# Kernel tuning notes

Hardware: AMD Instinct MI355X
Metric: run time of the kernel (lower is better)

Reference implementation:

```python
import jax, jax.numpy as jnp
import numpy as np

D_MODEL, D_STATE, D_INNER, DT_RANK, K = 64, 16, 128, 4, 4
EPS = 1e-6  # RMSNorm eps


def setup_inputs() -> dict:
    key = jax.random.key(0)
    ks = jax.random.split(key, 12)
    B, L = 8, 4096
    s = 0.02
    x = jax.random.normal(ks[0], (B, L, D_MODEL), dtype=jnp.float32)
    w_norm = jnp.ones((D_MODEL,), jnp.float32)
    W_in = jax.random.normal(ks[1], (2 * D_INNER, D_MODEL), jnp.float32) * s
    b_in = jnp.zeros((2 * D_INNER,), jnp.float32)
    W_conv = jax.random.normal(ks[2], (D_INNER, D_INNER, K), jnp.float32) * s
    b_conv = jnp.zeros((D_INNER,), jnp.float32)
    W_xp = jax.random.normal(ks[3], (DT_RANK + 2 * D_STATE, D_INNER), jnp.float32) * s
    b_xp = jnp.zeros((DT_RANK + 2 * D_STATE,), jnp.float32)
    W_dt = jax.random.normal(ks[4], (D_INNER, DT_RANK), jnp.float32) * s
    b_dt = jnp.zeros((D_INNER,), jnp.float32)
    W_out = jax.random.normal(ks[5], (D_MODEL, D_INNER), jnp.float32) * s
    b_out = jnp.zeros((D_MODEL,), jnp.float32)
    A_log = jnp.log(jnp.tile(jnp.arange(1, D_STATE + 1, dtype=jnp.float32), (D_INNER, 1)))
    D_param = jnp.ones((D_INNER,), jnp.float32)
    return dict(x=x, w_norm=w_norm, W_in=W_in, b_in=b_in, W_conv=W_conv, b_conv=b_conv,
                W_xp=W_xp, b_xp=b_xp, W_dt=W_dt, b_dt=b_dt, W_out=W_out, b_out=b_out,
                A_log=A_log, D_param=D_param)


def _mamba_block(xn, W_in, b_in, W_conv, b_conv, W_xp, b_xp, W_dt, b_dt, W_out, b_out, A_log, D_param):
    B, L, _ = xn.shape
    xz = xn @ W_in.T + b_in                      # (B,L,2*d_inner)
    u, z = jnp.split(xz, 2, axis=-1)
    z = jax.nn.silu(z)
    # conv1d: NCH, causal-style pad (K-1) both sides then truncate to L
    uc = jax.lax.conv_general_dilated(
        u.transpose(0, 2, 1), W_conv, window_strides=(1,), padding=[(K - 1, K - 1)],
        dimension_numbers=("NCH", "OIH", "NCH"))[:, :, :L] + b_conv[None, :, None]
    u = jax.nn.silu(uc.transpose(0, 2, 1))       # (B,L,d_inner)
    xp = u @ W_xp.T + b_xp
    dt, Bm, Cm = jnp.split(xp, [DT_RANK, DT_RANK + D_STATE], axis=-1)
    delta = jax.nn.softplus(dt @ W_dt.T + b_dt)  # (B,L,d_inner)
    A = -jnp.exp(A_log)                          # (d_inner, n)
    A_bar = jnp.exp(jnp.einsum('bld,dn->bldn', delta, A))
    B_bar_x = jnp.einsum('bld,bln,bld->bldn', delta, Bm, u)

    def step(h, inp):
        a, bx, c = inp                           # (B,d,n),(B,d,n),(B,n)
        h = a * h + bx
        y = jnp.einsum('bdn,bn->bd', h, c)
        return h, y

    h0 = jnp.zeros((B, D_INNER, D_STATE), xn.dtype)
    xs = (A_bar.transpose(1, 0, 2, 3), B_bar_x.transpose(1, 0, 2, 3), Cm.transpose(1, 0, 2))
    _, ys = jax.lax.scan(step, h0, xs)           # (L,B,d_inner)
    y = ys.transpose(1, 0, 2) + D_param * u
    y = y * z
    return y @ W_out.T + b_out


def reference(x, w_norm, W_in, b_in, W_conv, b_conv, W_xp, b_xp, W_dt, b_dt, W_out, b_out, A_log, D_param):
    xn = x * jax.lax.rsqrt(jnp.mean(x * x, axis=-1, keepdims=True) + EPS) * w_norm
    return x + _mamba_block(xn, W_in, b_in, W_conv, b_conv, W_xp, b_xp, W_dt, b_dt, W_out, b_out, A_log, D_param)
```

## Files before the change

### kernel.cpp

```cpp
#include <hip/hip_runtime.h>
#include <math.h>

#define D_MODEL 64
#define D_STATE 16
#define D_INNER 128
#define DT_RANK 4
#define BB 8
#define LL 4096
#define NTOK (BB*LL)
#define EPSV 1e-6f
#define NCHUNK 64
#define LC (LL/NCHUNK)
#define PAD 136

typedef __attribute__((ext_vector_type(8))) short bf16x8;
typedef __attribute__((ext_vector_type(4))) float f32x4;

__device__ __forceinline__ float sig_(float v) { return 1.f / (1.f + __expf(-v)); }
__device__ __forceinline__ float softplus_(float v) {
    return (v > 20.f) ? v : __logf(1.f + __expf(v));
}
__device__ __forceinline__ unsigned short f2bf(float x) {
    unsigned int u = __float_as_uint(x);
    u += 0x7fff + ((u >> 16) & 1);
    return (unsigned short)(u >> 16);
}
__device__ __forceinline__ float bf2f(unsigned short u) {
    return __uint_as_float(((unsigned int)u) << 16);
}
__device__ __forceinline__ unsigned int pack2bf(float a, float b) {
    return (unsigned int)f2bf(a) | ((unsigned int)f2bf(b) << 16);
}

__global__ __launch_bounds__(256) void pack_all(
    const float* __restrict__ W_in, const float* __restrict__ w_norm,
    const float* __restrict__ W_conv, const float* __restrict__ W_xp,
    const float* __restrict__ W_out,
    unsigned short* __restrict__ Win_bf, unsigned short* __restrict__ Bp,
    unsigned short* __restrict__ Wxp_bf, unsigned short* __restrict__ Wout_bf)
{
    int i = blockIdx.x * 256 + threadIdx.x;
    if (i < 16384) {
        Win_bf[i] = f2bf(W_in[i] * w_norm[i & 63]);
    } else if (i < 81920) {
        int j = i - 16384;
        int kk = j >> 14, o = (j >> 7) & 127, c = j & 127;
        Bp[j] = f2bf(W_conv[o * 512 + c * 4 + kk]);
    } else if (i < 88064) {
        int j = i - 81920;
        Wxp_bf[j] = ((j >> 7) < 36) ? f2bf(W_xp[j]) : (unsigned short)0;
    } else if (i < 96256) {
        int j = i - 88064;
        Wout_bf[j] = f2bf(W_out[j]);
    }
}

__global__ __launch_bounds__(256) void k1_fused(
    const float* __restrict__ x, const unsigned short* __restrict__ Win_bf,
    const float* __restrict__ b_in,
    unsigned short* __restrict__ u_bf, unsigned short* __restrict__ z_bf)
{
    __shared__ unsigned short axs[64 * 72];
    int tid = threadIdx.x;
    int tb = blockIdx.x * 64;
    {
        int t = tid >> 2, qt = tid & 3;
        float4 v[4];
        float ss = 0.f;
        #pragma unroll
        for (int j = 0; j < 4; ++j) {
            v[j] = *(const float4*)&x[(tb + t) * 64 + qt * 16 + j * 4];
            ss += v[j].x*v[j].x + v[j].y*v[j].y + v[j].z*v[j].z + v[j].w*v[j].w;
        }
        ss += __shfl_xor(ss, 1, 64);
        ss += __shfl_xor(ss, 2, 64);
        float r = rsqrtf(ss * (1.f / 64.f) + EPSV);
        unsigned short tmp[16];
        #pragma unroll
        for (int j = 0; j < 4; ++j) {
            tmp[4*j+0] = f2bf(v[j].x * r); tmp[4*j+1] = f2bf(v[j].y * r);
            tmp[4*j+2] = f2bf(v[j].z * r); tmp[4*j+3] = f2bf(v[j].w * r);
        }
        *(bf16x8*)&axs[t * 72 + qt * 16]     = *(bf16x8*)&tmp[0];
        *(bf16x8*)&axs[t * 72 + qt * 16 + 8] = *(bf16x8*)&tmp[8];
    }
    __syncthreads();
    int wave = tid >> 6, lane = tid & 63;
    int quad = lane >> 4, l16 = lane & 15;
    f32x4 acc[16];
    #pragma unroll
    for (int nt = 0; nt < 16; ++nt) acc[nt] = (f32x4){0.f, 0.f, 0.f, 0.f};
    bf16x8 a0 = *(const bf16x8*)&axs[(wave * 16 + l16) * 72 + quad * 8];
    bf16x8 a1 = *(const bf16x8*)&axs[(wave * 16 + l16) * 72 + 32 + quad * 8];
    #pragma unroll
    for (int nt = 0; nt < 16; ++nt) {
        bf16x8 b0 = *(const bf16x8*)&Win_bf[(nt * 16 + l16) * 64 + quad * 8];
        bf16x8 b1 = *(const bf16x8*)&Win_bf[(nt * 16 + l16) * 64 + 32 + quad * 8];
        acc[nt] = __builtin_amdgcn_mfma_f32_16x16x32_bf16(a0, b0, acc[nt], 0, 0, 0);
        acc[nt] = __builtin_amdgcn_mfma_f32_16x16x32_bf16(a1, b1, acc[nt], 0, 0, 0);
    }
    #pragma unroll
    for (int nt = 0; nt < 16; ++nt) {
        int o = nt * 16 + l16;
        float bo = b_in[o];
        #pragma unroll
        for (int r = 0; r < 4; ++r) {
            int t = tb + wave * 16 + quad * 4 + r;
            float v = acc[nt][r] + bo;
            if (o < 128) u_bf[t * 128 + o] = f2bf(v);
            else         z_bf[t * 128 + (o - 128)] = f2bf(v * sig_(v));
        }
    }
}

__global__ __launch_bounds__(256) void k2k3a_fused(
    const unsigned short* __restrict__ u_bf, const unsigned short* __restrict__ Bp,
    const float* __restrict__ b_conv,
    const unsigned short* __restrict__ Wxp_bf, const float* __restrict__ b_xp,
    const float* __restrict__ W_dt, const float* __restrict__ b_dt,
    const float* __restrict__ A_log,
    unsigned short* __restrict__ u_cbf, unsigned short* __restrict__ delta_bf,
    float* __restrict__ Bm, float* __restrict__ Cm,
    float* __restrict__ P, float* __restrict__ Q)
{
    __shared__ unsigned short uls[64 * PAD];
    __shared__ unsigned short dls[64 * PAD];
    __shared__ float bls[64 * 16];
    __shared__ float dts[64][4];
    __shared__ float Wd[512];
    __shared__ float bds[128];
    int tid = threadIdx.x;
    if (tid < 128) *(float4*)&Wd[tid * 4] = *(const float4*)&W_dt[tid * 4];
    else if (tid < 160) *(float4*)&bds[(tid - 128) * 4] = *(const float4*)&b_dt[(tid - 128) * 4];
    int wave = tid >> 6, lane = tid & 63;
    int quad = lane >> 4, l16 = lane & 15;
    int tb = blockIdx.x * 64;
    int bbase = tb & ~4095;
    int t0 = tb + wave * 16;
    f32x4 acc[8];
    #pragma unroll
    for (int og = 0; og < 8; ++og) acc[og] = (f32x4){0.f, 0.f, 0.f, 0.f};
    int row_base = t0 + l16 - 3;
    #pragma unroll
    for (int kk = 0; kk < 4; ++kk) {
        int row = row_base + kk;
        #pragma unroll
        for (int cs = 0; cs < 4; ++cs) {
            int kbase = cs * 32 + quad * 8;
            bf16x8 a = {0,0,0,0,0,0,0,0};
            if (row >= bbase)
                a = *(const bf16x8*)&u_bf[row * 128 + kbase];
            #pragma unroll
            for (int og = 0; og < 8; ++og) {
                bf16x8 b = *(const bf16x8*)&Bp[kk * 16384 + (og * 16 + l16) * 128 + kbase];
                acc[og] = __builtin_amdgcn_mfma_f32_16x16x32_bf16(a, b, acc[og], 0, 0, 0);
            }
        }
    }
    #pragma unroll
    for (int og = 0; og < 8; ++og) {
        int o = og * 16 + l16;
        float bc = b_conv[o];
        #pragma unroll
        for (int r = 0; r < 4; ++r) {
            int tloc = wave * 16 + quad * 4 + r;
            float v = acc[og][r] + bc;
            unsigned short ub = f2bf(v * sig_(v));
            u_cbf[(tb + tloc) * 128 + o] = ub;
            uls[tloc * PAD + o] = ub;
        }
    }
    __syncthreads();
    f32x4 xacc[3];
    #pragma unroll
    for (int nt = 0; nt < 3; ++nt) xacc[nt] = (f32x4){0.f, 0.f, 0.f, 0.f};
    #pragma unroll
    for (int cs = 0; cs < 4; ++cs) {
        int kbase = cs * 32 + quad * 8;
        bf16x8 a = *(const bf16x8*)&uls[(wave * 16 + l16) * PAD + kbase];
        #pragma unroll
        for (int nt = 0; nt < 3; ++nt) {
            bf16x8 b = *(const bf16x8*)&Wxp_bf[(nt * 16 + l16) * 128 + kbase];
            xacc[nt] = __builtin_amdgcn_mfma_f32_16x16x32_bf16(a, b, xacc[nt], 0, 0, 0);
        }
    }
    #pragma unroll
    for (int nt = 0; nt < 3; ++nt) {
        int j = nt * 16 + l16;
        float bx = (j < 36) ? b_xp[j] : 0.f;
        #pragma unroll
        for (int r = 0; r < 4; ++r) {
            int tloc = wave * 16 + quad * 4 + r;
            int t = tb + tloc;
            float val = xacc[nt][r] + bx;
            if (j < 4) {
                dts[tloc][j] = val;
            } else if (j < 20) {
                Bm[t * 16 + (j - 4)] = val;
                bls[tloc * 16 + (j - 4)] = val;
            } else if (j < 36) {
                Cm[t * 16 + (j - 20)] = val;
            }
        }
    }
    __syncthreads();
    {
        int tokloc = tid >> 2, dgrp = tid & 3;
        float dt0 = dts[tokloc][0], dt1 = dts[tokloc][1],
              dt2 = dts[tokloc][2], dt3 = dts[tokloc][3];
        int g = tb + tokloc;
        #pragma unroll
        for (int d4 = 0; d4 < 8; ++d4) {
            int d = dgrp * 32 + d4 * 4;
            float4 w0 = *(const float4*)&Wd[(d + 0) * 4];
            float4 w1 = *(const float4*)&Wd[(d + 1) * 4];
            float4 w2 = *(const float4*)&Wd[(d + 2) * 4];
            float4 w3 = *(const float4*)&Wd[(d + 3) * 4];
            float4 bdv = *(const float4*)&bds[d];
            float4 r;
            r.x = softplus_(bdv.x + dt0*w0.x + dt1*w0.y + dt2*w0.z + dt3*w0.w);
            r.y = softplus_(bdv.y + dt0*w1.x + dt1*w1.y + dt2*w1.z + dt3*w1.w);
            r.z = softplus_(bdv.z + dt0*w2.x + dt1*w2.y + dt2*w2.z + dt3*w2.w);
            r.w = softplus_(bdv.w + dt0*w3.x + dt1*w3.y + dt2*w3.z + dt3*w3.w);
            uint2 pk; pk.x = pack2bf(r.x, r.y); pk.y = pack2bf(r.z, r.w);
            *(uint2*)&delta_bf[g * 128 + d] = pk;
            *(uint2*)&dls[tokloc * PAD + d] = pk;
        }
    }
    __syncthreads();
    {
        int d = tid >> 1;
        int nb = (tid & 1) * 8;
        float4 Av0 = *(const float4*)&A_log[d * 16 + nb];
        float4 Av1 = *(const float4*)&A_log[d * 16 + nb + 4];
        float A0 = -__expf(Av0.x), A1 = -__expf(Av0.y),
              A2 = -__expf(Av0.z), A3 = -__expf(Av0.w);
        float A4 = -__expf(Av1.x), A5 = -__expf(Av1.y),
              A6 = -__expf(Av1.z), A7 = -__expf(Av1.w);
        float P0=1.f,P1=1.f,P2=1.f,P3=1.f,P4=1.f,P5=1.f,P6=1.f,P7=1.f;
        float Q0=0.f,Q1=0.f,Q2=0.f,Q3=0.f,Q4=0.f,Q5=0.f,Q6=0.f,Q7=0.f;
        for (int t = 0; t < LC; ++t) {
            float dl = bf2f(dls[t * PAD + d]);
            float uu = bf2f(uls[t * PAD + d]);
            float4 bm0 = *(const float4*)&bls[t * 16 + nb];
            float4 bm1 = *(const float4*)&bls[t * 16 + nb + 4];
            float du = dl * uu;
            float a0 = __expf(dl * A0), a1 = __expf(dl * A1),
                  a2 = __expf(dl * A2), a3 = __expf(dl * A3);
            float a4 = __expf(dl * A4), a5 = __expf(dl * A5),
                  a6 = __expf(dl * A6), a7 = __expf(dl * A7);
            P0 *= a0; P1 *= a1; P2 *= a2; P3 *= a3;
            P4 *= a4; P5 *= a5; P6 *= a6; P7 *= a7;
            Q0 = a0 * Q0 + du * bm0.x; Q1 = a1 * Q1 + du * bm0.y;
            Q2 = a2 * Q2 + du * bm0.z; Q3 = a3 * Q3 + du * bm0.w;
            Q4 = a4 * Q4 + du * bm1.x; Q5 = a5 * Q5 + du * bm1.y;
            Q6 = a6 * Q6 + du * bm1.z; Q7 = a7 * Q7 + du * bm1.w;
        }
        int idx = blockIdx.x * 2048 + d * 16 + nb;
        *(float4*)&P[idx]     = (float4){P0, P1, P2, P3};
        *(float4*)&P[idx + 4] = (float4){P4, P5, P6, P7};
        *(float4*)&Q[idx]     = (float4){Q0, Q1, Q2, Q3};
        *(float4*)&Q[idx + 4] = (float4){Q4, Q5, Q6, Q7};
    }
}

__global__ __launch_bounds__(256) void k4b_carry(
    const float* __restrict__ P, const float* __restrict__ Q, float* __restrict__ Hinit)
{
    int tid = blockIdx.x * 256 + threadIdx.x;
    int b = tid >> 11, dn = tid & 2047;
    float carry = 0.f;
    for (int c0 = 0; c0 < NCHUNK; c0 += 8) {
        float p[8], q[8];
        #pragma unroll
        for (int j = 0; j < 8; ++j) {
            int idx = (b * NCHUNK + c0 + j) * 2048 + dn;
            p[j] = P[idx]; q[j] = Q[idx];
        }
        #pragma unroll
        for (int j = 0; j < 8; ++j) {
            int idx = (b * NCHUNK + c0 + j) * 2048 + dn;
            Hinit[idx] = carry;
            carry = p[j] * carry + q[j];
        }
    }
}

__global__ __launch_bounds__(256) void k4c5_fused(
    const unsigned short* __restrict__ delta_bf, const unsigned short* __restrict__ u_cbf,
    const float* __restrict__ Bm, const float* __restrict__ Cm,
    const unsigned short* __restrict__ z_bf, const float* __restrict__ A_log,
    const float* __restrict__ D_param, const float* __restrict__ Hinit,
    const unsigned short* __restrict__ Wout_bf, const float* __restrict__ b_out,
    const float* __restrict__ x, float* __restrict__ out)
{
    __shared__ unsigned short dls[LC * 128];
    __shared__ unsigned short uls[LC * 128];
    __shared__ float bls[LC * 16];
    __shared__ float cls[LC * 16];
    __shared__ unsigned short yzls[LC * PAD];
    int bid = blockIdx.x;
    int tid = threadIdx.x, lane = tid & 63;
    int g0 = bid * 64;
    for (int i = tid; i < LC * 16; i += 256) {
        int row = i >> 4, q = i & 15;
        *(float4*)&dls[row * 128 + q * 8] =
            *(const float4*)&delta_bf[(g0 + row) * 128 + q * 8];
        *(float4*)&uls[row * 128 + q * 8] =
            *(const float4*)&u_cbf[(g0 + row) * 128 + q * 8];
        *(float4*)&yzls[row * PAD + q * 8] =
            *(const float4*)&z_bf[(g0 + row) * 128 + q * 8];
    }
    for (int i = tid; i < LC * 4; i += 256) {
        int row = i >> 2, q = i & 3;
        *(float4*)&bls[row * 16 + q * 4] = *(const float4*)&Bm[(g0 + row) * 16 + q * 4];
        *(float4*)&cls[row * 16 + q * 4] = *(const float4*)&Cm[(g0 + row) * 16 + q * 4];
    }
    int d = tid >> 1;
    int nb = (tid & 1) * 8;
    float4 Av0 = *(const float4*)&A_log[d * 16 + nb];
    float4 Av1 = *(const float4*)&A_log[d * 16 + nb + 4];
    float A0 = -__expf(Av0.x), A1 = -__expf(Av0.y), A2 = -__expf(Av0.z), A3 = -__expf(Av0.w);
    float A4 = -__expf(Av1.x), A5 = -__expf(Av1.y), A6 = -__expf(Av1.z), A7 = -__expf(Av1.w);
    int hbase = bid * 2048 + d * 16 + nb;
    float4 h0 = *(const float4*)&Hinit[hbase];
    float4 h1 = *(const float4*)&Hinit[hbase + 4];
    float Dp = D_param[d];
    __syncthreads();
    for (int t = 0; t < LC; ++t) {
        float dl = bf2f(dls[t * 128 + d]);
        float uu = bf2f(uls[t * 128 + d]);
        float4 bm0 = *(const float4*)&bls[t * 16 + nb];
        float4 bm1 = *(const float4*)&bls[t * 16 + nb + 4];
        float4 cm0 = *(const float4*)&cls[t * 16 + nb];
        float4 cm1 = *(const float4*)&cls[t * 16 + nb + 4];
        float du = dl * uu;
        float a0 = __expf(dl * A0), a1 = __expf(dl * A1),
              a2 = __expf(dl * A2), a3 = __expf(dl * A3);
        float a4 = __expf(dl * A4), a5 = __expf(dl * A5),
              a6 = __expf(dl * A6), a7 = __expf(dl * A7);
        h0.x = a0 * h0.x + du * bm0.x; h0.y = a1 * h0.y + du * bm0.y;
        h0.z = a2 * h0.z + du * bm0.z; h0.w = a3 * h0.w + du * bm0.w;
        h1.x = a4 * h1.x + du * bm1.x; h1.y = a5 * h1.y + du * bm1.y;
        h1.z = a6 * h1.z + du * bm1.z; h1.w = a7 * h1.w + du * bm1.w;
        float yv = h0.x * cm0.x + h0.y * cm0.y + h0.z * cm0.z + h0.w * cm0.w
                 + h1.x * cm1.x + h1.y * cm1.y + h1.z * cm1.z + h1.w * cm1.w;
        yv += __shfl_xor(yv, 1, 64);
        if ((tid & 1) == 0) {
            float y = yv + Dp * uu;
            y *= bf2f(yzls[t * PAD + d]);
            yzls[t * PAD + d] = f2bf(y);
        }
    }
    __syncthreads();
    int wave = tid >> 6;
    int quad = lane >> 4, l16 = lane & 15;
    f32x4 oacc[4];
    #pragma unroll
    for (int nt = 0; nt < 4; ++nt) oacc[nt] = (f32x4){0.f, 0.f, 0.f, 0.f};
    #pragma unroll
    for (int cs = 0; cs < 4; ++cs) {
        int kbase = cs * 32 + quad * 8;
        bf16x8 a = *(const bf16x8*)&yzls[(wave * 16 + l16) * PAD + kbase];
        #pragma unroll
        for (int nt = 0; nt < 4; ++nt) {
            bf16x8 bb = *(const bf16x8*)&Wout_bf[(nt * 16 + l16) * 128 + kbase];
            oacc[nt] = __builtin_amdgcn_mfma_f32_16x16x32_bf16(a, bb, oacc[nt], 0, 0, 0);
        }
    }
    #pragma unroll
    for (int nt = 0; nt < 4; ++nt) {
        int m = nt * 16 + l16;
        float bo = b_out[m];
        #pragma unroll
        for (int r = 0; r < 4; ++r) {
            int t = g0 + wave * 16 + quad * 4 + r;
            out[t * 64 + m] = oacc[nt][r] + bo + x[t * 64 + m];
        }
    }
}

extern "C" void kernel_launch(void* const* d_in, const int* in_sizes, int n_in,
                              void* d_out, int out_size, void* d_ws, size_t ws_size,
                              hipStream_t stream)
{
    const float* x       = (const float*)d_in[0];
    const float* w_norm  = (const float*)d_in[1];
    const float* W_in    = (const float*)d_in[2];
    const float* b_in    = (const float*)d_in[3];
    const float* W_conv  = (const float*)d_in[4];
    const float* b_conv  = (const float*)d_in[5];
    const float* W_xp    = (const float*)d_in[6];
    const float* b_xp    = (const float*)d_in[7];
    const float* W_dt    = (const float*)d_in[8];
    const float* b_dt    = (const float*)d_in[9];
    const float* W_out   = (const float*)d_in[10];
    const float* b_out   = (const float*)d_in[11];
    const float* A_log   = (const float*)d_in[12];
    const float* D_param = (const float*)d_in[13];
    float* ws = (float*)d_ws;

    unsigned short* u_bf = (unsigned short*)ws;
    unsigned short* z_bf = (unsigned short*)(ws + 2097152);
    unsigned short* u_cbf= (unsigned short*)(ws + 4194304);
    unsigned short* delta_bf = (unsigned short*)(ws + 6291456);
    float* Bm     = ws + 10485760;
    float* Cm     = ws + 11010048;
    float* P      = ws + 11534336;
    float* Q      = ws + 12582912;
    float* Hinit  = ws + 13631488;
    unsigned short* Bp      = (unsigned short*)(ws + 14680064);
    unsigned short* Wxp_bf  = (unsigned short*)(ws + 14712832);
    unsigned short* Wout_bf = (unsigned short*)(ws + 14715904);
    unsigned short* Win_bf  = (unsigned short*)(ws + 14720000);
    float* out    = (float*)d_out;

    pack_all<<<376, 256, 0, stream>>>(W_in, w_norm, W_conv, W_xp, W_out,
                                      Win_bf, Bp, Wxp_bf, Wout_bf);
    k1_fused<<<512, 256, 0, stream>>>(x, Win_bf, b_in, u_bf, z_bf);
    k2k3a_fused<<<512, 256, 0, stream>>>(u_bf, Bp, b_conv, Wxp_bf, b_xp,
                                         W_dt, b_dt, A_log,
                                         u_cbf, delta_bf, Bm, Cm, P, Q);
    k4b_carry<<<64, 256, 0, stream>>>(P, Q, Hinit);
    k4c5_fused<<<512, 256, 0, stream>>>(delta_bf, u_cbf, Bm, Cm, z_bf, A_log,
                                        D_param, Hinit, Wout_bf, b_out, x, out);
}
```

Baseline: 184.0 us.

## Double threads per block and split work across 8 waves in all main kernels

Raises block size from 256 to 512 threads in the three main kernels. Work is remapped so each wave covers half the output columns (GEMM tiles) and each scan thread handles 4 states instead of 8, with an extra shuffle reduction. The aim is more parallelism, since only 512 blocks are launched and the per-thread serial scan chains were long. The cost is more shuffles, more redundant A-fragment loads across waves, and uneven xp tile work between the two wave halves.

```diff
diff --git a/kernel.cpp b/kernel.cpp
--- a/kernel.cpp
+++ b/kernel.cpp
@@ -55,7 +55,7 @@
     }
 }
 
-__global__ __launch_bounds__(256) void k1_fused(
+__global__ __launch_bounds__(512) void k1_fused(
     const float* __restrict__ x, const unsigned short* __restrict__ Win_bf,
     const float* __restrict__ b_in,
     unsigned short* __restrict__ u_bf, unsigned short* __restrict__ z_bf)
@@ -64,56 +64,55 @@
     int tid = threadIdx.x;
     int tb = blockIdx.x * 64;
     {
-        int t = tid >> 2, qt = tid & 3;
-        float4 v[4];
-        float ss = 0.f;
-        #pragma unroll
-        for (int j = 0; j < 4; ++j) {
-            v[j] = *(const float4*)&x[(tb + t) * 64 + qt * 16 + j * 4];
-            ss += v[j].x*v[j].x + v[j].y*v[j].y + v[j].z*v[j].z + v[j].w*v[j].w;
-        }
+        int t = tid >> 3, p = tid & 7;
+        float4 v0 = *(const float4*)&x[(tb + t) * 64 + p * 8];
+        float4 v1 = *(const float4*)&x[(tb + t) * 64 + p * 8 + 4];
+        float ss = v0.x*v0.x + v0.y*v0.y + v0.z*v0.z + v0.w*v0.w
+                 + v1.x*v1.x + v1.y*v1.y + v1.z*v1.z + v1.w*v1.w;
         ss += __shfl_xor(ss, 1, 64);
         ss += __shfl_xor(ss, 2, 64);
+        ss += __shfl_xor(ss, 4, 64);
         float r = rsqrtf(ss * (1.f / 64.f) + EPSV);
-        unsigned short tmp[16];
-        #pragma unroll
-        for (int j = 0; j < 4; ++j) {
-            tmp[4*j+0] = f2bf(v[j].x * r); tmp[4*j+1] = f2bf(v[j].y * r);
-            tmp[4*j+2] = f2bf(v[j].z * r); tmp[4*j+3] = f2bf(v[j].w * r);
-        }
-        *(bf16x8*)&axs[t * 72 + qt * 16]     = *(bf16x8*)&tmp[0];
-        *(bf16x8*)&axs[t * 72 + qt * 16 + 8] = *(bf16x8*)&tmp[8];
+        unsigned short tmp[8];
+        tmp[0] = f2bf(v0.x * r); tmp[1] = f2bf(v0.y * r);
+        tmp[2] = f2bf(v0.z * r); tmp[3] = f2bf(v0.w * r);
+        tmp[4] = f2bf(v1.x * r); tmp[5] = f2bf(v1.y * r);
+        tmp[6] = f2bf(v1.z * r); tmp[7] = f2bf(v1.w * r);
+        *(bf16x8*)&axs[t * 72 + p * 8] = *(bf16x8*)&tmp[0];
     }
     __syncthreads();
     int wave = tid >> 6, lane = tid & 63;
     int quad = lane >> 4, l16 = lane & 15;
-    f32x4 acc[16];
-    #pragma unroll
-    for (int nt = 0; nt < 16; ++nt) acc[nt] = (f32x4){0.f, 0.f, 0.f, 0.f};
-    bf16x8 a0 = *(const bf16x8*)&axs[(wave * 16 + l16) * 72 + quad * 8];
-    bf16x8 a1 = *(const bf16x8*)&axs[(wave * 16 + l16) * 72 + 32 + quad * 8];
-    #pragma unroll
-    for (int nt = 0; nt < 16; ++nt) {
+    int tok16 = wave & 3;
+    int nth   = wave >> 2;
+    f32x4 acc[8];
+    #pragma unroll
+    for (int k = 0; k < 8; ++k) acc[k] = (f32x4){0.f, 0.f, 0.f, 0.f};
+    bf16x8 a0 = *(const bf16x8*)&axs[(tok16 * 16 + l16) * 72 + quad * 8];
+    bf16x8 a1 = *(const bf16x8*)&axs[(tok16 * 16 + l16) * 72 + 32 + quad * 8];
+    #pragma unroll
+    for (int k = 0; k < 8; ++k) {
+        int nt = nth * 8 + k;
         bf16x8 b0 = *(const bf16x8*)&Win_bf[(nt * 16 + l16) * 64 + quad * 8];
         bf16x8 b1 = *(const bf16x8*)&Win_bf[(nt * 16 + l16) * 64 + 32 + quad * 8];
-        acc[nt] = __builtin_amdgcn_mfma_f32_16x16x32_bf16(a0, b0, acc[nt], 0, 0, 0);
-        acc[nt] = __builtin_amdgcn_mfma_f32_16x16x32_bf16(a1, b1, acc[nt], 0, 0, 0);
-    }
-    #pragma unroll
-    for (int nt = 0; nt < 16; ++nt) {
-        int o = nt * 16 + l16;
+        acc[k] = __builtin_amdgcn_mfma_f32_16x16x32_bf16(a0, b0, acc[k], 0, 0, 0);
+        acc[k] = __builtin_amdgcn_mfma_f32_16x16x32_bf16(a1, b1, acc[k], 0, 0, 0);
+    }
+    #pragma unroll
+    for (int k = 0; k < 8; ++k) {
+        int o = (nth * 8 + k) * 16 + l16;
         float bo = b_in[o];
         #pragma unroll
         for (int r = 0; r < 4; ++r) {
-            int t = tb + wave * 16 + quad * 4 + r;
-            float v = acc[nt][r] + bo;
+            int t = tb + tok16 * 16 + quad * 4 + r;
+            float v = acc[k][r] + bo;
             if (o < 128) u_bf[t * 128 + o] = f2bf(v);
             else         z_bf[t * 128 + (o - 128)] = f2bf(v * sig_(v));
         }
     }
 }
 
-__global__ __launch_bounds__(256) void k2k3a_fused(
+__global__ __launch_bounds__(512) void k2k3a_fused(
     const unsigned short* __restrict__ u_bf, const unsigned short* __restrict__ Bp,
     const float* __restrict__ b_conv,
     const unsigned short* __restrict__ Wxp_bf, const float* __restrict__ b_xp,
@@ -136,10 +135,12 @@
     int quad = lane >> 4, l16 = lane & 15;
     int tb = blockIdx.x * 64;
     int bbase = tb & ~4095;
-    int t0 = tb + wave * 16;
-    f32x4 acc[8];
-    #pragma unroll
-    for (int og = 0; og < 8; ++og) acc[og] = (f32x4){0.f, 0.f, 0.f, 0.f};
+    int tok16 = wave & 3;
+    int ogh   = wave >> 2;
+    int t0 = tb + tok16 * 16;
+    f32x4 acc[4];
+    #pragma unroll
+    for (int og = 0; og < 4; ++og) acc[og] = (f32x4){0.f, 0.f, 0.f, 0.f};
     int row_base = t0 + l16 - 3;
     #pragma unroll
     for (int kk = 0; kk < 4; ++kk) {
@@ -151,19 +152,20 @@
             if (row >= bbase)
                 a = *(const bf16x8*)&u_bf[row * 128 + kbase];
             #pragma unroll
-            for (int og = 0; og < 8; ++og) {
-                bf16x8 b = *(const bf16x8*)&Bp[kk * 16384 + (og * 16 + l16) * 128 + kbase];
+            for (int og = 0; og < 4; ++og) {
+                int o16 = ogh * 4 + og;
+                bf16x8 b = *(const bf16x8*)&Bp[kk * 16384 + (o16 * 16 + l16) * 128 + kbase];
                 acc[og] = __builtin_amdgcn_mfma_f32_16x16x32_bf16(a, b, acc[og], 0, 0, 0);
             }
         }
     }
     #pragma unroll
-    for (int og = 0; og < 8; ++og) {
-        int o = og * 16 + l16;
+    for (int og = 0; og < 4; ++og) {
+        int o = (ogh * 4 + og) * 16 + l16;
         float bc = b_conv[o];
         #pragma unroll
         for (int r = 0; r < 4; ++r) {
-            int tloc = wave * 16 + quad * 4 + r;
+            int tloc = tok16 * 16 + quad * 4 + r;
             float v = acc[og][r] + bc;
             unsigned short ub = f2bf(v * sig_(v));
             u_cbf[(tb + tloc) * 128 + o] = ub;
@@ -171,47 +173,49 @@
         }
     }
     __syncthreads();
-    f32x4 xacc[3];
-    #pragma unroll
-    for (int nt = 0; nt < 3; ++nt) xacc[nt] = (f32x4){0.f, 0.f, 0.f, 0.f};
-    #pragma unroll
-    for (int cs = 0; cs < 4; ++cs) {
-        int kbase = cs * 32 + quad * 8;
-        bf16x8 a = *(const bf16x8*)&uls[(wave * 16 + l16) * PAD + kbase];
-        #pragma unroll
-        for (int nt = 0; nt < 3; ++nt) {
-            bf16x8 b = *(const bf16x8*)&Wxp_bf[(nt * 16 + l16) * 128 + kbase];
-            xacc[nt] = __builtin_amdgcn_mfma_f32_16x16x32_bf16(a, b, xacc[nt], 0, 0, 0);
-        }
-    }
-    #pragma unroll
-    for (int nt = 0; nt < 3; ++nt) {
-        int j = nt * 16 + l16;
-        float bx = (j < 36) ? b_xp[j] : 0.f;
-        #pragma unroll
-        for (int r = 0; r < 4; ++r) {
-            int tloc = wave * 16 + quad * 4 + r;
-            int t = tb + tloc;
-            float val = xacc[nt][r] + bx;
-            if (j < 4) {
-                dts[tloc][j] = val;
-            } else if (j < 20) {
-                Bm[t * 16 + (j - 4)] = val;
-                bls[tloc * 16 + (j - 4)] = val;
-            } else if (j < 36) {
-                Cm[t * 16 + (j - 20)] = val;
+    {
+        int nt0 = ogh * 2;
+        int ntc = 2 - ogh;
+        f32x4 xacc[2];
+        xacc[0] = (f32x4){0.f, 0.f, 0.f, 0.f};
+        xacc[1] = (f32x4){0.f, 0.f, 0.f, 0.f};
+        #pragma unroll
+        for (int cs = 0; cs < 4; ++cs) {
+            int kbase = cs * 32 + quad * 8;
+            bf16x8 a = *(const bf16x8*)&uls[(tok16 * 16 + l16) * PAD + kbase];
+            for (int k = 0; k < ntc; ++k) {
+                bf16x8 b = *(const bf16x8*)&Wxp_bf[((nt0 + k) * 16 + l16) * 128 + kbase];
+                xacc[k] = __builtin_amdgcn_mfma_f32_16x16x32_bf16(a, b, xacc[k], 0, 0, 0);
             }
         }
+        for (int k = 0; k < ntc; ++k) {
+            int j = (nt0 + k) * 16 + l16;
+            float bx = (j < 36) ? b_xp[j] : 0.f;
+            #pragma unroll
+            for (int r = 0; r < 4; ++r) {
+                int tloc = tok16 * 16 + quad * 4 + r;
+                int t = tb + tloc;
+                float val = xacc[k][r] + bx;
+                if (j < 4) {
+                    dts[tloc][j] = val;
+                } else if (j < 20) {
+                    Bm[t * 16 + (j - 4)] = val;
+                    bls[tloc * 16 + (j - 4)] = val;
+                } else if (j < 36) {
+                    Cm[t * 16 + (j - 20)] = val;
+                }
+            }
+        }
     }
     __syncthreads();
     {
-        int tokloc = tid >> 2, dgrp = tid & 3;
+        int tokloc = tid >> 3, dgrp = tid & 7;
         float dt0 = dts[tokloc][0], dt1 = dts[tokloc][1],
               dt2 = dts[tokloc][2], dt3 = dts[tokloc][3];
         int g = tb + tokloc;
         #pragma unroll
-        for (int d4 = 0; d4 < 8; ++d4) {
-            int d = dgrp * 32 + d4 * 4;
+        for (int d4 = 0; d4 < 4; ++d4) {
+            int d = dgrp * 16 + d4 * 4;
             float4 w0 = *(const float4*)&Wd[(d + 0) * 4];
             float4 w1 = *(const float4*)&Wd[(d + 1) * 4];
             float4 w2 = *(const float4*)&Wd[(d + 2) * 4];
@@ -229,38 +233,27 @@
     }
     __syncthreads();
     {
-        int d = tid >> 1;
-        int nb = (tid & 1) * 8;
-        float4 Av0 = *(const float4*)&A_log[d * 16 + nb];
-        float4 Av1 = *(const float4*)&A_log[d * 16 + nb + 4];
-        float A0 = -__expf(Av0.x), A1 = -__expf(Av0.y),
-              A2 = -__expf(Av0.z), A3 = -__expf(Av0.w);
-        float A4 = -__expf(Av1.x), A5 = -__expf(Av1.y),
-              A6 = -__expf(Av1.z), A7 = -__expf(Av1.w);
-        float P0=1.f,P1=1.f,P2=1.f,P3=1.f,P4=1.f,P5=1.f,P6=1.f,P7=1.f;
-        float Q0=0.f,Q1=0.f,Q2=0.f,Q3=0.f,Q4=0.f,Q5=0.f,Q6=0.f,Q7=0.f;
+        int d = tid >> 2;
+        int nb = (tid & 3) * 4;
+        float4 Av = *(const float4*)&A_log[d * 16 + nb];
+        float A0 = -__expf(Av.x), A1 = -__expf(Av.y),
+              A2 = -__expf(Av.z), A3 = -__expf(Av.w);
+        float P0=1.f,P1=1.f,P2=1.f,P3=1.f;
+        float Q0=0.f,Q1=0.f,Q2=0.f,Q3=0.f;
         for (int t = 0; t < LC; ++t) {
             float dl = bf2f(dls[t * PAD + d]);
             float uu = bf2f(uls[t * PAD + d]);
-            float4 bm0 = *(const float4*)&bls[t * 16 + nb];
-            float4 bm1 = *(const float4*)&bls[t * 16 + nb + 4];
+            float4 bm = *(const float4*)&bls[t * 16 + nb];
             float du = dl * uu;
             float a0 = __expf(dl * A0), a1 = __expf(dl * A1),
                   a2 = __expf(dl * A2), a3 = __expf(dl * A3);
-            float a4 = __expf(dl * A4), a5 = __expf(dl * A5),
-                  a6 = __expf(dl * A6), a7 = __expf(dl * A7);
             P0 *= a0; P1 *= a1; P2 *= a2; P3 *= a3;
-            P4 *= a4; P5 *= a5; P6 *= a6; P7 *= a7;
-            Q0 = a0 * Q0 + du * bm0.x; Q1 = a1 * Q1 + du * bm0.y;
-            Q2 = a2 * Q2 + du * bm0.z; Q3 = a3 * Q3 + du * bm0.w;
-            Q4 = a4 * Q4 + du * bm1.x; Q5 = a5 * Q5 + du * bm1.y;
-            Q6 = a6 * Q6 + du * bm1.z; Q7 = a7 * Q7 + du * bm1.w;
+            Q0 = a0 * Q0 + du * bm.x; Q1 = a1 * Q1 + du * bm.y;
+            Q2 = a2 * Q2 + du * bm.z; Q3 = a3 * Q3 + du * bm.w;
         }
         int idx = blockIdx.x * 2048 + d * 16 + nb;
-        *(float4*)&P[idx]     = (float4){P0, P1, P2, P3};
-        *(float4*)&P[idx + 4] = (float4){P4, P5, P6, P7};
-        *(float4*)&Q[idx]     = (float4){Q0, Q1, Q2, Q3};
-        *(float4*)&Q[idx + 4] = (float4){Q4, Q5, Q6, Q7};
+        *(float4*)&P[idx] = (float4){P0, P1, P2, P3};
+        *(float4*)&Q[idx] = (float4){Q0, Q1, Q2, Q3};
     }
 }
 
@@ -286,7 +279,7 @@
     }
 }
 
-__global__ __launch_bounds__(256) void k4c5_fused(
+__global__ __launch_bounds__(512) void k4c5_fused(
     const unsigned short* __restrict__ delta_bf, const unsigned short* __restrict__ u_cbf,
     const float* __restrict__ Bm, const float* __restrict__ Cm,
     const unsigned short* __restrict__ z_bf, const float* __restrict__ A_log,
@@ -302,7 +295,7 @@
     int bid = blockIdx.x;
     int tid = threadIdx.x, lane = tid & 63;
     int g0 = bid * 64;
-    for (int i = tid; i < LC * 16; i += 256) {
+    for (int i = tid; i < LC * 16; i += 512) {
         int row = i >> 4, q = i & 15;
         *(float4*)&dls[row * 128 + q * 8] =
             *(const float4*)&delta_bf[(g0 + row) * 128 + q * 8];
@@ -311,42 +304,32 @@
         *(float4*)&yzls[row * PAD + q * 8] =
             *(const float4*)&z_bf[(g0 + row) * 128 + q * 8];
     }
-    for (int i = tid; i < LC * 4; i += 256) {
-        int row = i >> 2, q = i & 3;
+    if (tid < LC * 4) {
+        int row = tid >> 2, q = tid & 3;
         *(float4*)&bls[row * 16 + q * 4] = *(const float4*)&Bm[(g0 + row) * 16 + q * 4];
         *(float4*)&cls[row * 16 + q * 4] = *(const float4*)&Cm[(g0 + row) * 16 + q * 4];
     }
-    int d = tid >> 1;
-    int nb = (tid & 1) * 8;
-    float4 Av0 = *(const float4*)&A_log[d * 16 + nb];
-    float4 Av1 = *(const float4*)&A_log[d * 16 + nb + 4];
-    float A0 = -__expf(Av0.x), A1 = -__expf(Av0.y), A2 = -__expf(Av0.z), A3 = -__expf(Av0.w);
-    float A4 = -__expf(Av1.x), A5 = -__expf(Av1.y), A6 = -__expf(Av1.z), A7 = -__expf(Av1.w);
-    int hbase = bid * 2048 + d * 16 + nb;
-    float4 h0 = *(const float4*)&Hinit[hbase];
-    float4 h1 = *(const float4*)&Hinit[hbase + 4];
+    int d = tid >> 2;
+    int nb = (tid & 3) * 4;
+    float4 Av = *(const float4*)&A_log[d * 16 + nb];
+    float A0 = -__expf(Av.x), A1 = -__expf(Av.y), A2 = -__expf(Av.z), A3 = -__expf(Av.w);
+    float4 h = *(const float4*)&Hinit[bid * 2048 + d * 16 + nb];
     float Dp = D_param[d];
     __syncthreads();
     for (int t = 0; t < LC; ++t) {
         float dl = bf2f(dls[t * 128 + d]);
         float uu = bf2f(uls[t * 128 + d]);
-        float4 bm0 = *(const float4*)&bls[t * 16 + nb];
-        float4 bm1 = *(const float4*)&bls[t * 16 + nb + 4];
-        float4 cm0 = *(const float4*)&cls[t * 16 + nb];
-        float4 cm1 = *(const float4*)&cls[t * 16 + nb + 4];
+        float4 bm = *(const float4*)&bls[t * 16 + nb];
+        float4 cm = *(const float4*)&cls[t * 16 + nb];
         float du = dl * uu;
         float a0 = __expf(dl * A0), a1 = __expf(dl * A1),
               a2 = __expf(dl * A2), a3 = __expf(dl * A3);
-        float a4 = __expf(dl * A4), a5 = __expf(dl * A5),
-              a6 = __expf(dl * A6), a7 = __expf(dl * A7);
-        h0.x = a0 * h0.x + du * bm0.x; h0.y = a1 * h0.y + du * bm0.y;
-        h0.z = a2 * h0.z + du * bm0.z; h0.w = a3 * h0.w + du * bm0.w;
-        h1.x = a4 * h1.x + du * bm1.x; h1.y = a5 * h1.y + du * bm1.y;
-        h1.z = a6 * h1.z + du * bm1.z; h1.w = a7 * h1.w + du * bm1.w;
-        float yv = h0.x * cm0.x + h0.y * cm0.y + h0.z * cm0.z + h0.w * cm0.w
-                 + h1.x * cm1.x + h1.y * cm1.y + h1.z * cm1.z + h1.w * cm1.w;
+        h.x = a0 * h.x + du * bm.x; h.y = a1 * h.y + du * bm.y;
+        h.z = a2 * h.z + du * bm.z; h.w = a3 * h.w + du * bm.w;
+        float yv = h.x * cm.x + h.y * cm.y + h.z * cm.z + h.w * cm.w;
         yv += __shfl_xor(yv, 1, 64);
-        if ((tid & 1) == 0) {
+        yv += __shfl_xor(yv, 2, 64);
+        if ((tid & 3) == 0) {
             float y = yv + Dp * uu;
             y *= bf2f(yzls[t * PAD + d]);
             yzls[t * PAD + d] = f2bf(y);
@@ -355,27 +338,29 @@
     __syncthreads();
     int wave = tid >> 6;
     int quad = lane >> 4, l16 = lane & 15;
-    f32x4 oacc[4];
-    #pragma unroll
-    for (int nt = 0; nt < 4; ++nt) oacc[nt] = (f32x4){0.f, 0.f, 0.f, 0.f};
+    int tok16 = wave & 3, grp = wave >> 2;
+    f32x4 oacc[2];
+    oacc[0] = (f32x4){0.f, 0.f, 0.f, 0.f};
+    oacc[1] = (f32x4){0.f, 0.f, 0.f, 0.f};
     #pragma unroll
     for (int cs = 0; cs < 4; ++cs) {
         int kbase = cs * 32 + quad * 8;
-        bf16x8 a = *(const bf16x8*)&yzls[(wave * 16 + l16) * PAD + kbase];
-        #pragma unroll
-        for (int nt = 0; nt < 4; ++nt) {
+        bf16x8 a = *(const bf16x8*)&yzls[(tok16 * 16 + l16) * PAD + kbase];
+        #pragma unroll
+        for (int k = 0; k < 2; ++k) {
+            int nt = grp * 2 + k;
             bf16x8 bb = *(const bf16x8*)&Wout_bf[(nt * 16 + l16) * 128 + kbase];
-            oacc[nt] = __builtin_amdgcn_mfma_f32_16x16x32_bf16(a, bb, oacc[nt], 0, 0, 0);
-        }
-    }
-    #pragma unroll
-    for (int nt = 0; nt < 4; ++nt) {
-        int m = nt * 16 + l16;
+            oacc[k] = __builtin_amdgcn_mfma_f32_16x16x32_bf16(a, bb, oacc[k], 0, 0, 0);
+        }
+    }
+    #pragma unroll
+    for (int k = 0; k < 2; ++k) {
+        int m = (grp * 2 + k) * 16 + l16;
         float bo = b_out[m];
         #pragma unroll
         for (int r = 0; r < 4; ++r) {
-            int t = g0 + wave * 16 + quad * 4 + r;
-            out[t * 64 + m] = oacc[nt][r] + bo + x[t * 64 + m];
+            int t = g0 + tok16 * 16 + quad * 4 + r;
+            out[t * 64 + m] = oacc[k][r] + bo + x[t * 64 + m];
         }
     }
 }
@@ -417,11 +402,11 @@
 
     pack_all<<<376, 256, 0, stream>>>(W_in, w_norm, W_conv, W_xp, W_out,
                                       Win_bf, Bp, Wxp_bf, Wout_bf);
-    k1_fused<<<512, 256, 0, stream>>>(x, Win_bf, b_in, u_bf, z_bf);
-    k2k3a_fused<<<512, 256, 0, stream>>>(u_bf, Bp, b_conv, Wxp_bf, b_xp,
+    k1_fused<<<512, 512, 0, stream>>>(x, Win_bf, b_in, u_bf, z_bf);
+    k2k3a_fused<<<512, 512, 0, stream>>>(u_bf, Bp, b_conv, Wxp_bf, b_xp,
                                          W_dt, b_dt, A_log,
                                          u_cbf, delta_bf, Bm, Cm, P, Q);
     k4b_carry<<<64, 256, 0, stream>>>(P, Q, Hinit);
-    k4c5_fused<<<512, 256, 0, stream>>>(delta_bf, u_cbf, Bm, Cm, z_bf, A_log,
+    k4c5_fused<<<512, 512, 0, stream>>>(delta_bf, u_cbf, Bm, Cm, z_bf, A_log,
                                         D_param, Hinit, Wout_bf, b_out, x, out);
 }
```

Result: slower. 191.3 us (+4.0%).

## Halve scan chunk length to double block count for conv and scan kernels

Applied to the files above, without the earlier changes.

Doubles the number of scan chunks so each block of the conv/x-proj and scan/out-proj kernels handles 32 tokens instead of 64, launching 1024 blocks instead of 512. Waves are remapped so that two waves share a 16-token tile and split the output columns between them. This aims for better occupancy and shorter serial scan chunks. In exchange, the P/Q carry arrays double in size, the carry kernel has more chunks to combine, and each block does less work relative to its fixed weight-loading overhead.

```diff
diff --git a/kernel.cpp b/kernel.cpp
--- a/kernel.cpp
+++ b/kernel.cpp
@@ -9,7 +9,7 @@
 #define LL 4096
 #define NTOK (BB*LL)
 #define EPSV 1e-6f
-#define NCHUNK 64
+#define NCHUNK 128
 #define LC (LL/NCHUNK)
 #define PAD 136
 
@@ -123,10 +123,10 @@
     float* __restrict__ Bm, float* __restrict__ Cm,
     float* __restrict__ P, float* __restrict__ Q)
 {
-    __shared__ unsigned short uls[64 * PAD];
-    __shared__ unsigned short dls[64 * PAD];
-    __shared__ float bls[64 * 16];
-    __shared__ float dts[64][4];
+    __shared__ unsigned short uls[32 * PAD];
+    __shared__ unsigned short dls[32 * PAD];
+    __shared__ float bls[32 * 16];
+    __shared__ float dts[32][4];
     __shared__ float Wd[512];
     __shared__ float bds[128];
     int tid = threadIdx.x;
@@ -134,12 +134,14 @@
     else if (tid < 160) *(float4*)&bds[(tid - 128) * 4] = *(const float4*)&b_dt[(tid - 128) * 4];
     int wave = tid >> 6, lane = tid & 63;
     int quad = lane >> 4, l16 = lane & 15;
-    int tb = blockIdx.x * 64;
+    int tb = blockIdx.x * 32;
     int bbase = tb & ~4095;
-    int t0 = tb + wave * 16;
-    f32x4 acc[8];
-    #pragma unroll
-    for (int og = 0; og < 8; ++og) acc[og] = (f32x4){0.f, 0.f, 0.f, 0.f};
+    int tok16 = wave & 1;
+    int ogh   = wave >> 1;
+    int t0 = tb + tok16 * 16;
+    f32x4 acc[4];
+    #pragma unroll
+    for (int og = 0; og < 4; ++og) acc[og] = (f32x4){0.f, 0.f, 0.f, 0.f};
     int row_base = t0 + l16 - 3;
     #pragma unroll
     for (int kk = 0; kk < 4; ++kk) {
@@ -151,19 +153,20 @@
             if (row >= bbase)
                 a = *(const bf16x8*)&u_bf[row * 128 + kbase];
             #pragma unroll
-            for (int og = 0; og < 8; ++og) {
-                bf16x8 b = *(const bf16x8*)&Bp[kk * 16384 + (og * 16 + l16) * 128 + kbase];
+            for (int og = 0; og < 4; ++og) {
+                int o16 = ogh * 4 + og;
+                bf16x8 b = *(const bf16x8*)&Bp[kk * 16384 + (o16 * 16 + l16) * 128 + kbase];
                 acc[og] = __builtin_amdgcn_mfma_f32_16x16x32_bf16(a, b, acc[og], 0, 0, 0);
             }
         }
     }
     #pragma unroll
-    for (int og = 0; og < 8; ++og) {
-        int o = og * 16 + l16;
+    for (int og = 0; og < 4; ++og) {
+        int o = (ogh * 4 + og) * 16 + l16;
         float bc = b_conv[o];
         #pragma unroll
         for (int r = 0; r < 4; ++r) {
-            int tloc = wave * 16 + quad * 4 + r;
+            int tloc = tok16 * 16 + quad * 4 + r;
             float v = acc[og][r] + bc;
             unsigned short ub = f2bf(v * sig_(v));
             u_cbf[(tb + tloc) * 128 + o] = ub;
@@ -171,47 +174,49 @@
         }
     }
     __syncthreads();
-    f32x4 xacc[3];
-    #pragma unroll
-    for (int nt = 0; nt < 3; ++nt) xacc[nt] = (f32x4){0.f, 0.f, 0.f, 0.f};
-    #pragma unroll
-    for (int cs = 0; cs < 4; ++cs) {
-        int kbase = cs * 32 + quad * 8;
-        bf16x8 a = *(const bf16x8*)&uls[(wave * 16 + l16) * PAD + kbase];
-        #pragma unroll
-        for (int nt = 0; nt < 3; ++nt) {
-            bf16x8 b = *(const bf16x8*)&Wxp_bf[(nt * 16 + l16) * 128 + kbase];
-            xacc[nt] = __builtin_amdgcn_mfma_f32_16x16x32_bf16(a, b, xacc[nt], 0, 0, 0);
-        }
-    }
-    #pragma unroll
-    for (int nt = 0; nt < 3; ++nt) {
-        int j = nt * 16 + l16;
-        float bx = (j < 36) ? b_xp[j] : 0.f;
-        #pragma unroll
-        for (int r = 0; r < 4; ++r) {
-            int tloc = wave * 16 + quad * 4 + r;
-            int t = tb + tloc;
-            float val = xacc[nt][r] + bx;
-            if (j < 4) {
-                dts[tloc][j] = val;
-            } else if (j < 20) {
-                Bm[t * 16 + (j - 4)] = val;
-                bls[tloc * 16 + (j - 4)] = val;
-            } else if (j < 36) {
-                Cm[t * 16 + (j - 20)] = val;
+    {
+        int nt0 = ogh * 2;
+        int ntc = 2 - ogh;
+        f32x4 xacc[2];
+        xacc[0] = (f32x4){0.f, 0.f, 0.f, 0.f};
+        xacc[1] = (f32x4){0.f, 0.f, 0.f, 0.f};
+        #pragma unroll
+        for (int cs = 0; cs < 4; ++cs) {
+            int kbase = cs * 32 + quad * 8;
+            bf16x8 a = *(const bf16x8*)&uls[(tok16 * 16 + l16) * PAD + kbase];
+            for (int k = 0; k < ntc; ++k) {
+                bf16x8 b = *(const bf16x8*)&Wxp_bf[((nt0 + k) * 16 + l16) * 128 + kbase];
+                xacc[k] = __builtin_amdgcn_mfma_f32_16x16x32_bf16(a, b, xacc[k], 0, 0, 0);
             }
         }
+        for (int k = 0; k < ntc; ++k) {
+            int j = (nt0 + k) * 16 + l16;
+            float bx = (j < 36) ? b_xp[j] : 0.f;
+            #pragma unroll
+            for (int r = 0; r < 4; ++r) {
+                int tloc = tok16 * 16 + quad * 4 + r;
+                int t = tb + tloc;
+                float val = xacc[k][r] + bx;
+                if (j < 4) {
+                    dts[tloc][j] = val;
+                } else if (j < 20) {
+                    Bm[t * 16 + (j - 4)] = val;
+                    bls[tloc * 16 + (j - 4)] = val;
+                } else if (j < 36) {
+                    Cm[t * 16 + (j - 20)] = val;
+                }
+            }
+        }
     }
     __syncthreads();
     {
-        int tokloc = tid >> 2, dgrp = tid & 3;
+        int tokloc = tid >> 3, dgrp = tid & 7;
         float dt0 = dts[tokloc][0], dt1 = dts[tokloc][1],
               dt2 = dts[tokloc][2], dt3 = dts[tokloc][3];
         int g = tb + tokloc;
         #pragma unroll
-        for (int d4 = 0; d4 < 8; ++d4) {
-            int d = dgrp * 32 + d4 * 4;
+        for (int d4 = 0; d4 < 4; ++d4) {
+            int d = dgrp * 16 + d4 * 4;
             float4 w0 = *(const float4*)&Wd[(d + 0) * 4];
             float4 w1 = *(const float4*)&Wd[(d + 1) * 4];
             float4 w2 = *(const float4*)&Wd[(d + 2) * 4];
@@ -301,7 +306,7 @@
     __shared__ unsigned short yzls[LC * PAD];
     int bid = blockIdx.x;
     int tid = threadIdx.x, lane = tid & 63;
-    int g0 = bid * 64;
+    int g0 = bid * 32;
     for (int i = tid; i < LC * 16; i += 256) {
         int row = i >> 4, q = i & 15;
         *(float4*)&dls[row * 128 + q * 8] =
@@ -311,8 +316,8 @@
         *(float4*)&yzls[row * PAD + q * 8] =
             *(const float4*)&z_bf[(g0 + row) * 128 + q * 8];
     }
-    for (int i = tid; i < LC * 4; i += 256) {
-        int row = i >> 2, q = i & 3;
+    if (tid < LC * 4) {
+        int row = tid >> 2, q = tid & 3;
         *(float4*)&bls[row * 16 + q * 4] = *(const float4*)&Bm[(g0 + row) * 16 + q * 4];
         *(float4*)&cls[row * 16 + q * 4] = *(const float4*)&Cm[(g0 + row) * 16 + q * 4];
     }
@@ -355,27 +360,29 @@
     __syncthreads();
     int wave = tid >> 6;
     int quad = lane >> 4, l16 = lane & 15;
-    f32x4 oacc[4];
-    #pragma unroll
-    for (int nt = 0; nt < 4; ++nt) oacc[nt] = (f32x4){0.f, 0.f, 0.f, 0.f};
+    int tok16 = wave & 1, grp = wave >> 1;
+    f32x4 oacc[2];
+    oacc[0] = (f32x4){0.f, 0.f, 0.f, 0.f};
+    oacc[1] = (f32x4){0.f, 0.f, 0.f, 0.f};
     #pragma unroll
     for (int cs = 0; cs < 4; ++cs) {
         int kbase = cs * 32 + quad * 8;
-        bf16x8 a = *(const bf16x8*)&yzls[(wave * 16 + l16) * PAD + kbase];
-        #pragma unroll
-        for (int nt = 0; nt < 4; ++nt) {
+        bf16x8 a = *(const bf16x8*)&yzls[(tok16 * 16 + l16) * PAD + kbase];
+        #pragma unroll
+        for (int k = 0; k < 2; ++k) {
+            int nt = grp * 2 + k;
             bf16x8 bb = *(const bf16x8*)&Wout_bf[(nt * 16 + l16) * 128 + kbase];
-            oacc[nt] = __builtin_amdgcn_mfma_f32_16x16x32_bf16(a, bb, oacc[nt], 0, 0, 0);
-        }
-    }
-    #pragma unroll
-    for (int nt = 0; nt < 4; ++nt) {
-        int m = nt * 16 + l16;
+            oacc[k] = __builtin_amdgcn_mfma_f32_16x16x32_bf16(a, bb, oacc[k], 0, 0, 0);
+        }
+    }
+    #pragma unroll
+    for (int k = 0; k < 2; ++k) {
+        int m = (grp * 2 + k) * 16 + l16;
         float bo = b_out[m];
         #pragma unroll
         for (int r = 0; r < 4; ++r) {
-            int t = g0 + wave * 16 + quad * 4 + r;
-            out[t * 64 + m] = oacc[nt][r] + bo + x[t * 64 + m];
+            int t = g0 + tok16 * 16 + quad * 4 + r;
+            out[t * 64 + m] = oacc[k][r] + bo + x[t * 64 + m];
         }
     }
 }
@@ -404,24 +411,24 @@
     unsigned short* z_bf = (unsigned short*)(ws + 2097152);
     unsigned short* u_cbf= (unsigned short*)(ws + 4194304);
     unsigned short* delta_bf = (unsigned short*)(ws + 6291456);
-    float* Bm     = ws + 10485760;
-    float* Cm     = ws + 11010048;
-    float* P      = ws + 11534336;
-    float* Q      = ws + 12582912;
+    float* Bm     = ws + 8388608;
+    float* Cm     = ws + 8912896;
+    float* P      = ws + 9437184;
+    float* Q      = ws + 11534336;
     float* Hinit  = ws + 13631488;
-    unsigned short* Bp      = (unsigned short*)(ws + 14680064);
-    unsigned short* Wxp_bf  = (unsigned short*)(ws + 14712832);
-    unsigned short* Wout_bf = (unsigned short*)(ws + 14715904);
-    unsigned short* Win_bf  = (unsigned short*)(ws + 14720000);
+    unsigned short* Bp      = (unsigned short*)(ws + 15728640);
+    unsigned short* Wxp_bf  = (unsigned short*)(ws + 15761408);
+    unsigned short* Wout_bf = (unsigned short*)(ws + 15765504);
+    unsigned short* Win_bf  = (unsigned short*)(ws + 15769600);
     float* out    = (float*)d_out;
 
     pack_all<<<376, 256, 0, stream>>>(W_in, w_norm, W_conv, W_xp, W_out,
                                       Win_bf, Bp, Wxp_bf, Wout_bf);
     k1_fused<<<512, 256, 0, stream>>>(x, Win_bf, b_in, u_bf, z_bf);
-    k2k3a_fused<<<512, 256, 0, stream>>>(u_bf, Bp, b_conv, Wxp_bf, b_xp,
-                                         W_dt, b_dt, A_log,
-                                         u_cbf, delta_bf, Bm, Cm, P, Q);
+    k2k3a_fused<<<1024, 256, 0, stream>>>(u_bf, Bp, b_conv, Wxp_bf, b_xp,
+                                          W_dt, b_dt, A_log,
+                                          u_cbf, delta_bf, Bm, Cm, P, Q);
     k4b_carry<<<64, 256, 0, stream>>>(P, Q, Hinit);
-    k4c5_fused<<<512, 256, 0, stream>>>(delta_bf, u_cbf, Bm, Cm, z_bf, A_log,
-                                        D_param, Hinit, Wout_bf, b_out, x, out);
-}
+    k4c5_fused<<<1024, 256, 0, stream>>>(delta_bf, u_cbf, Bm, Cm, z_bf, A_log,
+                                         D_param, Hinit, Wout_bf, b_out, x, out);
+}
```

New measurement: 188.8 us. 1.03x slower.
